# Performance work log

Hardware: AMD Instinct MI355X
Metric: run time of the kernel (lower is better)

The kernel has to match this reference:

```python
import jax, jax.numpy as jnp
import numpy as np

HIDDEN = 1024
ATT = 512

def _xavier(key, shape):
    fan_in, fan_out = shape[0], shape[1]
    bound = float(np.sqrt(6.0 / (fan_in + fan_out)))
    return jax.random.uniform(key, shape, jnp.float32, -bound, bound)

def setup_inputs() -> dict:
    key = jax.random.key(0)
    ks = jax.random.split(key, 7)
    B, P = 256, 196
    spatial_image = jax.random.normal(ks[0], (B, P, HIDDEN), jnp.float32)
    decoder_out = jax.random.normal(ks[1], (B, HIDDEN), jnp.float32)
    st = jax.random.normal(ks[2], (B, HIDDEN), jnp.float32)
    # weights stored as (in_dim, out_dim); math identical to torch Linear(x @ W.T)
    W_cnn = _xavier(ks[3], (HIDDEN, ATT))
    W_dec = _xavier(ks[4], (HIDDEN, ATT))
    W_sen = _xavier(ks[5], (HIDDEN, ATT))
    W_att = _xavier(ks[6], (ATT, 1))
    return {"spatial_image": spatial_image, "decoder_out": decoder_out, "st": st,
            "W_cnn": W_cnn, "W_dec": W_dec, "W_sen": W_sen, "W_att": W_att}

def reference(spatial_image, decoder_out, st, W_cnn, W_dec, W_sen, W_att):
    # dropout in eval mode (identity)
    cnn_out = jnp.einsum('bph,ha->bpa', spatial_image, W_cnn)   # (B,P,A)
    dec_out = decoder_out @ W_dec                                # (B,A)
    addition = jnp.tanh(cnn_out + dec_out[:, None, :])           # (B,P,A)
    zt = jnp.einsum('bpa,a->bp', addition, W_att[:, 0])          # (B,P)
    alpha_t = jax.nn.softmax(zt, axis=1)                         # (B,P)
    ct = jnp.einsum('bph,bp->bh', spatial_image, alpha_t)        # (B,H)
    sen = jnp.tanh(dec_out + st @ W_sen)                         # (B,A)
    out = sen @ W_att                                            # (B,1)
    concat = jnp.concatenate([zt, out], axis=1)                  # (B,P+1)
    alpha_hat = jax.nn.softmax(concat, axis=1)
    beta_t = alpha_hat[:, -1:]                                   # (B,1)
    c_hat = beta_t * st + (1.0 - beta_t) * ct                    # (B,H)
    return (alpha_t, beta_t, c_hat)
```

## Files before the change

### kernel.cpp

```cpp
#include <hip/hip_runtime.h>
#include <hip/hip_bf16.h>

#define BATCH   256
#define NP      196
#define HIDDEN  1024
#define ATT     512
#define M_TOTAL (BATCH * NP)

typedef __attribute__((ext_vector_type(8))) short bf16x8v;
typedef __attribute__((ext_vector_type(4))) float f32x4;

__device__ inline unsigned short f2bf(float x) {
    unsigned int u = __float_as_uint(x);
    u += 0x7fffu + ((u >> 16) & 1u);
    return (unsigned short)(u >> 16);
}

__device__ inline float fast_tanh(float x) {
    float e = __expf(2.0f * x);
    return 1.0f - 2.0f / (e + 1.0f);
}

__global__ void k0_arrange(const float* __restrict__ Wc, unsigned short* __restrict__ Wt) {
    int g = blockIdx.x * 256 + threadIdx.x;
    int kt    = g >> 11;
    int slot  = g & 2047;
    int chunk = slot >> 9;
    int n     = slot & 511;
    int kb = kt * 32 + chunk * 8;
    unsigned short v[8];
#pragma unroll
    for (int j = 0; j < 8; ++j) v[j] = f2bf(Wc[(kb + j) * ATT + n]);
    uint4 pk;
    pk.x = (unsigned int)v[0] | ((unsigned int)v[1] << 16);
    pk.y = (unsigned int)v[2] | ((unsigned int)v[3] << 16);
    pk.z = (unsigned int)v[4] | ((unsigned int)v[5] << 16);
    pk.w = (unsigned int)v[6] | ((unsigned int)v[7] << 16);
    *(uint4*)(Wt + (size_t)g * 8) = pk;
}

__global__ void k1_small(const float* __restrict__ dec_in, const float* __restrict__ st,
                         const float* __restrict__ Wdec,  const float* __restrict__ Wsen,
                         float* __restrict__ dec_out, float* __restrict__ stw) {
    const float* X = blockIdx.z ? st   : dec_in;
    const float* W = blockIdx.z ? Wsen : Wdec;
    float*       O = blockIdx.z ? stw  : dec_out;
    int ci = threadIdx.x & 31;
    int c0 = blockIdx.x * 128 + ci * 4;
    int b  = blockIdx.y * 8 + (threadIdx.x >> 5);
    const float* x = X + (size_t)b * HIDDEN;
    float4 acc = {0.f, 0.f, 0.f, 0.f};
    for (int k = 0; k < HIDDEN; k += 4) {
#pragma unroll
        for (int kk = 0; kk < 4; ++kk) {
            float4 w = *(const float4*)(W + (size_t)(k + kk) * ATT + c0);
            float a = x[k + kk];
            acc.x += a * w.x; acc.y += a * w.y; acc.z += a * w.z; acc.w += a * w.w;
        }
    }
    *(float4*)(O + (size_t)b * ATT + c0) = acc;
}

__global__ void __launch_bounds__(512)
k2_fused_gemm(const float* __restrict__ A, const unsigned short* __restrict__ Wt,
              const float* __restrict__ dec, const float* __restrict__ Watt,
              float* __restrict__ zt) {
    __shared__ __align__(16) unsigned short Abuf[4 * 64 * 8];
    __shared__ __align__(16) unsigned short Bbuf[4 * 512 * 8];
    __shared__ float zred[64 * 8];

    const int tid = threadIdx.x;
    const int w = tid >> 6;
    const int l = tid & 63;
    const int lg = l >> 4, ll = l & 15;
    const int r0 = blockIdx.x * 64;

    f32x4 acc[4][4];
#pragma unroll
    for (int m = 0; m < 4; ++m)
#pragma unroll
        for (int n = 0; n < 4; ++n) acc[m][n] = (f32x4){0.f, 0.f, 0.f, 0.f};

    const int arow = tid >> 3;
    const int akp  = tid & 7;
    const float* aptr = A + (size_t)(r0 + arow) * HIDDEN + akp * 4;
    const int aslot = (((akp >> 1) * 64 + arow) << 3) + (akp & 1) * 4;

    for (int kt = 0; kt < 32; ++kt) {
        float4 av = *(const float4*)(aptr + kt * 32);
        const uint4* bsrc = (const uint4*)(Wt + (size_t)kt * 16384);
        uint4 bv0 = bsrc[tid];
        uint4 bv1 = bsrc[512 + tid];
        uint4 bv2 = bsrc[1024 + tid];
        uint4 bv3 = bsrc[1536 + tid];

        __syncthreads();

        uint2 pk;
        pk.x = (unsigned int)f2bf(av.x) | ((unsigned int)f2bf(av.y) << 16);
        pk.y = (unsigned int)f2bf(av.z) | ((unsigned int)f2bf(av.w) << 16);
        *(uint2*)(Abuf + aslot) = pk;
        ((uint4*)Bbuf)[tid]        = bv0;
        ((uint4*)Bbuf)[512 + tid]  = bv1;
        ((uint4*)Bbuf)[1024 + tid] = bv2;
        ((uint4*)Bbuf)[1536 + tid] = bv3;

        __syncthreads();

        bf16x8v af[4], bfr[4];
#pragma unroll
        for (int m = 0; m < 4; ++m)
            af[m] = *(const bf16x8v*)(Abuf + ((lg * 64 + m * 16 + ll) << 3));
#pragma unroll
        for (int n = 0; n < 4; ++n)
            bfr[n] = *(const bf16x8v*)(Bbuf + ((lg * 512 + w * 64 + n * 16 + ll) << 3));
#pragma unroll
        for (int m = 0; m < 4; ++m)
#pragma unroll
            for (int n = 0; n < 4; ++n)
                acc[m][n] = __builtin_amdgcn_mfma_f32_16x16x32_bf16(af[m], bfr[n], acc[m][n], 0, 0, 0);
    }

    const int colb = w * 64 + ll;
    float watt[4];
#pragma unroll
    for (int n = 0; n < 4; ++n) watt[n] = Watt[colb + n * 16];

#pragma unroll
    for (int m = 0; m < 4; ++m) {
#pragma unroll
        for (int j = 0; j < 4; ++j) {
            int rl = m * 16 + lg * 4 + j;
            int rowg = r0 + rl;
            int b = rowg / NP;
            const float* db = dec + (size_t)b * ATT;
            float s = 0.f;
#pragma unroll
            for (int n = 0; n < 4; ++n)
                s += fast_tanh(acc[m][n][j] + db[colb + n * 16]) * watt[n];
            s += __shfl_xor(s, 1);
            s += __shfl_xor(s, 2);
            s += __shfl_xor(s, 4);
            s += __shfl_xor(s, 8);
            if (ll == 0) zred[rl * 8 + w] = s;
        }
    }
    __syncthreads();
    if (tid < 64) {
        float t = 0.f;
#pragma unroll
        for (int j = 0; j < 8; ++j) t += zred[tid * 8 + j];
        zt[r0 + tid] = t;
    }
}

__global__ void k3_softmax(const float* __restrict__ dec, const float* __restrict__ stw,
                           const float* __restrict__ Watt, const float* __restrict__ zt,
                           float* __restrict__ out, float* __restrict__ beta_ws) {
    int b = blockIdx.x;
    int t = threadIdx.x;
    __shared__ float red[256];

    float p = 0.f;
#pragma unroll
    for (int c = t; c < ATT; c += 256)
        p += fast_tanh(dec[(size_t)b * ATT + c] + stw[(size_t)b * ATT + c]) * Watt[c];
    red[t] = p;
    __syncthreads();
    for (int s = 128; s > 0; s >>= 1) { if (t < s) red[t] += red[t + s]; __syncthreads(); }
    float outv = red[0];
    __syncthreads();

    float z = (t < NP) ? zt[b * NP + t] : -1e30f;
    red[t] = z;
    __syncthreads();
    for (int s = 128; s > 0; s >>= 1) { if (t < s) red[t] = fmaxf(red[t], red[t + s]); __syncthreads(); }
    float m1 = red[0];
    __syncthreads();

    float e = (t < NP) ? __expf(z - m1) : 0.f;
    red[t] = e;
    __syncthreads();
    for (int s = 128; s > 0; s >>= 1) { if (t < s) red[t] += red[t + s]; __syncthreads(); }
    float s1 = red[0];

    if (t < NP) out[b * NP + t] = e / s1;

    if (t == 0) {
        float m2 = fmaxf(m1, outv);
        float s2 = s1 * __expf(m1 - m2) + __expf(outv - m2);
        float beta = __expf(outv - m2) / s2;
        out[M_TOTAL + b] = beta;
        beta_ws[b] = beta;
    }
}

__global__ void k4_ct(const float* __restrict__ spatial, const float* __restrict__ alpha,
                      float* __restrict__ ctp) {
    int q = blockIdx.x;
    int b = blockIdx.y;
    int t = threadIdx.x;
    __shared__ float al[49];
    if (t < 49) al[t] = alpha[b * NP + q * 49 + t];
    __syncthreads();
    const float* sp = spatial + (size_t)b * NP * HIDDEN + (size_t)q * 49 * HIDDEN + t * 4;
    float4 acc = {0.f, 0.f, 0.f, 0.f};
#pragma unroll 7
    for (int p = 0; p < 49; ++p) {
        float4 v = *(const float4*)(sp + (size_t)p * HIDDEN);
        float a = al[p];
        acc.x += a * v.x; acc.y += a * v.y; acc.z += a * v.z; acc.w += a * v.w;
    }
    *(float4*)(ctp + ((size_t)q * BATCH + b) * HIDDEN + t * 4) = acc;
}

__global__ void k5_chat(const float* __restrict__ st, const float* __restrict__ ctp,
                        const float* __restrict__ beta, float* __restrict__ chat) {
    int g = blockIdx.x * 256 + threadIdx.x;
    int b = g >> 8;
    int h0 = (g & 255) * 4;
    float be = beta[b];
    float4 s = *(const float4*)(st + (size_t)b * HIDDEN + h0);
    float4 c = {0.f, 0.f, 0.f, 0.f};
#pragma unroll
    for (int q = 0; q < 4; ++q) {
        float4 v = *(const float4*)(ctp + ((size_t)q * BATCH + b) * HIDDEN + h0);
        c.x += v.x; c.y += v.y; c.z += v.z; c.w += v.w;
    }
    float4 o;
    o.x = be * s.x + (1.f - be) * c.x;
    o.y = be * s.y + (1.f - be) * c.y;
    o.z = be * s.z + (1.f - be) * c.z;
    o.w = be * s.w + (1.f - be) * c.w;
    *(float4*)(chat + (size_t)b * HIDDEN + h0) = o;
}

extern "C" void kernel_launch(void* const* d_in, const int* in_sizes, int n_in,
                              void* d_out, int out_size, void* d_ws, size_t ws_size,
                              hipStream_t stream) {
    const float* spatial = (const float*)d_in[0];
    const float* decoder = (const float*)d_in[1];
    const float* st      = (const float*)d_in[2];
    const float* Wcnn    = (const float*)d_in[3];
    const float* Wdec    = (const float*)d_in[4];
    const float* Wsen    = (const float*)d_in[5];
    const float* Watt    = (const float*)d_in[6];
    float* out = (float*)d_out;

    char* ws = (char*)d_ws;
    unsigned short* Wt  = (unsigned short*)(ws + 0);
    float* zt   = (float*)(ws + 1048576);
    float* dec  = (float*)(ws + 1249280);
    float* stw  = (float*)(ws + 1773568);
    float* beta = (float*)(ws + 2297856);
    float* ctp  = (float*)(ws + 2298880);

    k0_arrange<<<256, 256, 0, stream>>>(Wcnn, Wt);
    k1_small<<<dim3(4, 32, 2), 256, 0, stream>>>(decoder, st, Wdec, Wsen, dec, stw);
    k2_fused_gemm<<<784, 512, 0, stream>>>(spatial, Wt, dec, Watt, zt);
    k3_softmax<<<256, 256, 0, stream>>>(dec, stw, Watt, zt, out, beta);
    k4_ct<<<dim3(4, 256), 256, 0, stream>>>(spatial, out, ctp);
    k5_chat<<<256, 256, 0, stream>>>(st, ctp, beta, out + M_TOTAL + BATCH);
}
```

Baseline: 192.5 us.

## Retile fused GEMM to 128x256 with direct-to-LDS B loads and split-N partial logits

The fused GEMM moves from 64-row tiles spanning all 512 attention columns to 128x256 tiles on a 2x4 wave grid. The weight is rearranged per column half, and partial logits for each half are written separately, then summed in the softmax kernel. B tiles go straight from global memory to LDS via global_load_lds. A loads are prefetched one k-step ahead and converted with a packed bf16 instruction. A block-index swizzle groups tiles for L2 locality. The intent is less LDS staging traffic, more A reuse per weight load, and latency hiding, at the cost of an extra partial-logit buffer and tighter occupancy bounds.

```diff
diff --git a/kernel.cpp b/kernel.cpp
--- a/kernel.cpp
+++ b/kernel.cpp
@@ -6,6 +6,11 @@
 #define HIDDEN  1024
 #define ATT     512
 #define M_TOTAL (BATCH * NP)
+#define BM 128
+#define BN 256
+#define BK 32
+#define MT_TILES (M_TOTAL / BM)
+#define NB_TILES (ATT / BN)
 
 typedef __attribute__((ext_vector_type(8))) short bf16x8v;
 typedef __attribute__((ext_vector_type(4))) float f32x4;
@@ -16,21 +21,36 @@
     return (unsigned short)(u >> 16);
 }
 
+__device__ __forceinline__ unsigned int pk2bf(float lo, float hi) {
+    unsigned int r;
+    asm("v_cvt_pk_bf16_f32 %0, %1, %2" : "=v"(r) : "v"(lo), "v"(hi));
+    return r;
+}
+
 __device__ inline float fast_tanh(float x) {
     float e = __expf(2.0f * x);
     return 1.0f - 2.0f / (e + 1.0f);
 }
 
+__device__ __forceinline__ void glds16(const void* gsrc, void* ldst) {
+    __builtin_amdgcn_global_load_lds(
+        (const __attribute__((address_space(1))) unsigned int*)gsrc,
+        (__attribute__((address_space(3))) unsigned int*)ldst,
+        16, 0, 0);
+}
+
 __global__ void k0_arrange(const float* __restrict__ Wc, unsigned short* __restrict__ Wt) {
     int g = blockIdx.x * 256 + threadIdx.x;
-    int kt    = g >> 11;
-    int slot  = g & 2047;
-    int chunk = slot >> 9;
-    int n     = slot & 511;
-    int kb = kt * 32 + chunk * 8;
+    int nb    = g >> 15;
+    int rem   = g & 32767;
+    int kt    = rem >> 10;
+    int chunk = (rem >> 8) & 3;
+    int n     = rem & 255;
+    int col   = nb * 256 + n;
+    int kb    = kt * 32 + chunk * 8;
     unsigned short v[8];
 #pragma unroll
-    for (int j = 0; j < 8; ++j) v[j] = f2bf(Wc[(kb + j) * ATT + n]);
+    for (int j = 0; j < 8; ++j) v[j] = f2bf(Wc[(size_t)(kb + j) * ATT + col]);
     uint4 pk;
     pk.x = (unsigned int)v[0] | ((unsigned int)v[1] << 16);
     pk.y = (unsigned int)v[2] | ((unsigned int)v[3] << 16);
@@ -61,19 +81,25 @@
     *(float4*)(O + (size_t)b * ATT + c0) = acc;
 }
 
-__global__ void __launch_bounds__(512)
+__global__ void __launch_bounds__(512, 4)
 k2_fused_gemm(const float* __restrict__ A, const unsigned short* __restrict__ Wt,
               const float* __restrict__ dec, const float* __restrict__ Watt,
-              float* __restrict__ zt) {
-    __shared__ __align__(16) unsigned short Abuf[4 * 64 * 8];
-    __shared__ __align__(16) unsigned short Bbuf[4 * 512 * 8];
-    __shared__ float zred[64 * 8];
+              float* __restrict__ ztp) {
+    __shared__ __align__(16) unsigned short Abuf[4 * 128 * 8];
+    __shared__ __align__(16) unsigned short Bbuf[4 * 256 * 8];
+    __shared__ float zred[128 * 4];
 
     const int tid = threadIdx.x;
-    const int w = tid >> 6;
-    const int l = tid & 63;
+    const int w  = tid >> 6;
+    const int l  = tid & 63;
     const int lg = l >> 4, ll = l & 15;
-    const int r0 = blockIdx.x * 64;
+    const int wr = w >> 2, wc = w & 3;
+
+    const int bid = (int)blockIdx.x;
+    const int swz = (bid & 7) * 98 + (bid >> 3);
+    const int mt = swz >> 1, nb = swz & 1;
+    const int r0 = mt * BM;
+    const int c0 = nb * BN;
 
     f32x4 acc[4][4];
 #pragma unroll
@@ -81,39 +107,47 @@
 #pragma unroll
         for (int n = 0; n < 4; ++n) acc[m][n] = (f32x4){0.f, 0.f, 0.f, 0.f};
 
-    const int arow = tid >> 3;
-    const int akp  = tid & 7;
-    const float* aptr = A + (size_t)(r0 + arow) * HIDDEN + akp * 4;
-    const int aslot = (((akp >> 1) * 64 + arow) << 3) + (akp & 1) * 4;
+    const int arow = tid >> 2;
+    const int ach  = tid & 3;
+    const float* aptr = A + (size_t)(r0 + arow) * HIDDEN + ach * 8;
+    unsigned short* aslot = Abuf + (ach * 128 + arow) * 8;
+
+    const size_t wt_base = (size_t)nb * 32 * 8192;
+    const char* bsrc0 = (const char*)(Wt + wt_base) + (w * 2 + 0) * 1024 + l * 16;
+    const char* bsrc1 = (const char*)(Wt + wt_base) + (w * 2 + 1) * 1024 + l * 16;
+    char* bdst0 = (char*)Bbuf + (w * 2 + 0) * 1024 + l * 16;
+    char* bdst1 = (char*)Bbuf + (w * 2 + 1) * 1024 + l * 16;
+
+    float4 a0 = *(const float4*)(aptr);
+    float4 a1 = *(const float4*)(aptr + 4);
 
     for (int kt = 0; kt < 32; ++kt) {
-        float4 av = *(const float4*)(aptr + kt * 32);
-        const uint4* bsrc = (const uint4*)(Wt + (size_t)kt * 16384);
-        uint4 bv0 = bsrc[tid];
-        uint4 bv1 = bsrc[512 + tid];
-        uint4 bv2 = bsrc[1024 + tid];
-        uint4 bv3 = bsrc[1536 + tid];
-
         __syncthreads();
 
-        uint2 pk;
-        pk.x = (unsigned int)f2bf(av.x) | ((unsigned int)f2bf(av.y) << 16);
-        pk.y = (unsigned int)f2bf(av.z) | ((unsigned int)f2bf(av.w) << 16);
-        *(uint2*)(Abuf + aslot) = pk;
-        ((uint4*)Bbuf)[tid]        = bv0;
-        ((uint4*)Bbuf)[512 + tid]  = bv1;
-        ((uint4*)Bbuf)[1024 + tid] = bv2;
-        ((uint4*)Bbuf)[1536 + tid] = bv3;
+        glds16(bsrc0 + kt * 16384, bdst0);
+        glds16(bsrc1 + kt * 16384, bdst1);
+
+        uint4 ap;
+        ap.x = pk2bf(a0.x, a0.y);
+        ap.y = pk2bf(a0.z, a0.w);
+        ap.z = pk2bf(a1.x, a1.y);
+        ap.w = pk2bf(a1.z, a1.w);
+        *(uint4*)aslot = ap;
 
         __syncthreads();
 
+        if (kt < 31) {
+            a0 = *(const float4*)(aptr + (kt + 1) * 32);
+            a1 = *(const float4*)(aptr + (kt + 1) * 32 + 4);
+        }
+
         bf16x8v af[4], bfr[4];
 #pragma unroll
         for (int m = 0; m < 4; ++m)
-            af[m] = *(const bf16x8v*)(Abuf + ((lg * 64 + m * 16 + ll) << 3));
+            af[m] = *(const bf16x8v*)(Abuf + ((lg * 128 + wr * 64 + m * 16 + ll) << 3));
 #pragma unroll
         for (int n = 0; n < 4; ++n)
-            bfr[n] = *(const bf16x8v*)(Bbuf + ((lg * 512 + w * 64 + n * 16 + ll) << 3));
+            bfr[n] = *(const bf16x8v*)(Bbuf + ((lg * 256 + wc * 64 + n * 16 + ll) << 3));
 #pragma unroll
         for (int m = 0; m < 4; ++m)
 #pragma unroll
@@ -121,41 +155,39 @@
                 acc[m][n] = __builtin_amdgcn_mfma_f32_16x16x32_bf16(af[m], bfr[n], acc[m][n], 0, 0, 0);
     }
 
-    const int colb = w * 64 + ll;
+    const int clocal = wc * 64 + ll;
     float watt[4];
 #pragma unroll
-    for (int n = 0; n < 4; ++n) watt[n] = Watt[colb + n * 16];
+    for (int n = 0; n < 4; ++n) watt[n] = Watt[c0 + clocal + n * 16];
 
 #pragma unroll
     for (int m = 0; m < 4; ++m) {
 #pragma unroll
         for (int j = 0; j < 4; ++j) {
-            int rl = m * 16 + lg * 4 + j;
+            int rl = wr * 64 + m * 16 + lg * 4 + j;
             int rowg = r0 + rl;
             int b = rowg / NP;
-            const float* db = dec + (size_t)b * ATT;
+            const float* db = dec + (size_t)b * ATT + c0;
             float s = 0.f;
 #pragma unroll
             for (int n = 0; n < 4; ++n)
-                s += fast_tanh(acc[m][n][j] + db[colb + n * 16]) * watt[n];
+                s += fast_tanh(acc[m][n][j] + db[clocal + n * 16]) * watt[n];
             s += __shfl_xor(s, 1);
             s += __shfl_xor(s, 2);
             s += __shfl_xor(s, 4);
             s += __shfl_xor(s, 8);
-            if (ll == 0) zred[rl * 8 + w] = s;
+            if (ll == 0) zred[rl * 4 + wc] = s;
         }
     }
     __syncthreads();
-    if (tid < 64) {
-        float t = 0.f;
-#pragma unroll
-        for (int j = 0; j < 8; ++j) t += zred[tid * 8 + j];
-        zt[r0 + tid] = t;
+    if (tid < 128) {
+        float t = zred[tid * 4] + zred[tid * 4 + 1] + zred[tid * 4 + 2] + zred[tid * 4 + 3];
+        ztp[(size_t)nb * M_TOTAL + r0 + tid] = t;
     }
 }
 
 __global__ void k3_softmax(const float* __restrict__ dec, const float* __restrict__ stw,
-                           const float* __restrict__ Watt, const float* __restrict__ zt,
+                           const float* __restrict__ Watt, const float* __restrict__ ztp,
                            float* __restrict__ out, float* __restrict__ beta_ws) {
     int b = blockIdx.x;
     int t = threadIdx.x;
@@ -171,7 +203,8 @@
     float outv = red[0];
     __syncthreads();
 
-    float z = (t < NP) ? zt[b * NP + t] : -1e30f;
+    float z = -1e30f;
+    if (t < NP) z = ztp[b * NP + t] + ztp[M_TOTAL + b * NP + t];
     red[t] = z;
     __syncthreads();
     for (int s = 128; s > 0; s >>= 1) { if (t < s) red[t] = fmaxf(red[t], red[t + s]); __syncthreads(); }
@@ -248,17 +281,17 @@
     float* out = (float*)d_out;
 
     char* ws = (char*)d_ws;
-    unsigned short* Wt  = (unsigned short*)(ws + 0);
-    float* zt   = (float*)(ws + 1048576);
-    float* dec  = (float*)(ws + 1249280);
-    float* stw  = (float*)(ws + 1773568);
-    float* beta = (float*)(ws + 2297856);
-    float* ctp  = (float*)(ws + 2298880);
+    unsigned short* Wt = (unsigned short*)(ws + 0);
+    float* ztp  = (float*)(ws + 1048576);
+    float* dec  = (float*)(ws + 1449984);
+    float* stw  = (float*)(ws + 1974272);
+    float* beta = (float*)(ws + 2498560);
+    float* ctp  = (float*)(ws + 2499584);
 
     k0_arrange<<<256, 256, 0, stream>>>(Wcnn, Wt);
     k1_small<<<dim3(4, 32, 2), 256, 0, stream>>>(decoder, st, Wdec, Wsen, dec, stw);
-    k2_fused_gemm<<<784, 512, 0, stream>>>(spatial, Wt, dec, Watt, zt);
-    k3_softmax<<<256, 256, 0, stream>>>(dec, stw, Watt, zt, out, beta);
+    k2_fused_gemm<<<MT_TILES * NB_TILES, 512, 0, stream>>>(spatial, Wt, dec, Watt, ztp);
+    k3_softmax<<<256, 256, 0, stream>>>(dec, stw, Watt, ztp, out, beta);
     k4_ct<<<dim3(4, 256), 256, 0, stream>>>(spatial, out, ctp);
     k5_chat<<<256, 256, 0, stream>>>(st, ctp, beta, out + M_TOTAL + BATCH);
 }
```

Result: faster. 186.2 us (-3.3%).

## Restructure fused GEMM: resident A tile in LDS, double-buffered async B loads

Applied to the files above, without the earlier changes.

The main GEMM kernel now loads the full 64x1024 A row tile once, converts it to bf16 with packed conversions, and keeps it resident in a swizzled 128KB LDS region. The N dimension is split into two 256-column halves processed sequentially by 4 waves, and B tiles are streamed with global_load_lds into double buffers so loads overlap MFMA work. It also adds a block-index remap, XOR swizzles to avoid bank conflicts, and s_setprio around MFMAs. The aim is to remove per-iteration A reloads and register-staged B copies, at the cost of one block per CU due to the large LDS footprint.

```diff
diff --git a/kernel.cpp b/kernel.cpp
--- a/kernel.cpp
+++ b/kernel.cpp
@@ -6,6 +6,8 @@
 #define HIDDEN  1024
 #define ATT     512
 #define M_TOTAL (BATCH * NP)
+#define BM 64
+#define MT_TILES (M_TOTAL / BM)
 
 typedef __attribute__((ext_vector_type(8))) short bf16x8v;
 typedef __attribute__((ext_vector_type(4))) float f32x4;
@@ -16,21 +18,36 @@
     return (unsigned short)(u >> 16);
 }
 
+__device__ __forceinline__ unsigned int pk2bf(float lo, float hi) {
+    unsigned int r;
+    asm("v_cvt_pk_bf16_f32 %0, %1, %2" : "=v"(r) : "v"(lo), "v"(hi));
+    return r;
+}
+
 __device__ inline float fast_tanh(float x) {
     float e = __expf(2.0f * x);
     return 1.0f - 2.0f / (e + 1.0f);
 }
 
+__device__ __forceinline__ void glds16(const void* gsrc, void* ldst) {
+    __builtin_amdgcn_global_load_lds(
+        (const __attribute__((address_space(1))) unsigned int*)gsrc,
+        (__attribute__((address_space(3))) unsigned int*)ldst,
+        16, 0, 0);
+}
+
 __global__ void k0_arrange(const float* __restrict__ Wc, unsigned short* __restrict__ Wt) {
     int g = blockIdx.x * 256 + threadIdx.x;
-    int kt    = g >> 11;
-    int slot  = g & 2047;
-    int chunk = slot >> 9;
-    int n     = slot & 511;
-    int kb = kt * 32 + chunk * 8;
+    int h    = g >> 15;
+    int kt   = (g >> 10) & 31;
+    int col  = (g >> 2) & 255;
+    int slot = g & 3;
+    int c    = slot ^ ((col >> 1) & 3);
+    int kb   = kt * 32 + c * 8;
+    int colg = h * 256 + col;
     unsigned short v[8];
 #pragma unroll
-    for (int j = 0; j < 8; ++j) v[j] = f2bf(Wc[(kb + j) * ATT + n]);
+    for (int j = 0; j < 8; ++j) v[j] = f2bf(Wc[(size_t)(kb + j) * ATT + colg]);
     uint4 pk;
     pk.x = (unsigned int)v[0] | ((unsigned int)v[1] << 16);
     pk.y = (unsigned int)v[2] | ((unsigned int)v[3] << 16);
@@ -61,96 +78,152 @@
     *(float4*)(O + (size_t)b * ATT + c0) = acc;
 }
 
-__global__ void __launch_bounds__(512)
-k2_fused_gemm(const float* __restrict__ A, const unsigned short* __restrict__ Wt,
-              const float* __restrict__ dec, const float* __restrict__ Watt,
-              float* __restrict__ zt) {
-    __shared__ __align__(16) unsigned short Abuf[4 * 64 * 8];
-    __shared__ __align__(16) unsigned short Bbuf[4 * 512 * 8];
-    __shared__ float zred[64 * 8];
+__global__ void __launch_bounds__(256, 1)
+k2_fused(const float* __restrict__ A, const unsigned short* __restrict__ Wt,
+         const float* __restrict__ dec, const float* __restrict__ Watt,
+         float* __restrict__ zt) {
+    __shared__ __align__(16) char lds[163840];
+    char* B0 = lds + 131072;
+    char* B1 = lds + 147456;
+    float* zred = (float*)(lds + 131072);
 
     const int tid = threadIdx.x;
-    const int w = tid >> 6;
-    const int l = tid & 63;
+    const int wv = tid >> 6;
+    const int l  = tid & 63;
     const int lg = l >> 4, ll = l & 15;
-    const int r0 = blockIdx.x * 64;
+
+    const int bid = (int)blockIdx.x;
+    const int mt = (bid & 7) * 98 + (bid >> 3);
+    const int r0 = mt * BM;
 
     f32x4 acc[4][4];
 #pragma unroll
     for (int m = 0; m < 4; ++m)
 #pragma unroll
         for (int n = 0; n < 4; ++n) acc[m][n] = (f32x4){0.f, 0.f, 0.f, 0.f};
-
-    const int arow = tid >> 3;
-    const int akp  = tid & 7;
-    const float* aptr = A + (size_t)(r0 + arow) * HIDDEN + akp * 4;
-    const int aslot = (((akp >> 1) * 64 + arow) << 3) + (akp & 1) * 4;
-
-    for (int kt = 0; kt < 32; ++kt) {
-        float4 av = *(const float4*)(aptr + kt * 32);
-        const uint4* bsrc = (const uint4*)(Wt + (size_t)kt * 16384);
-        uint4 bv0 = bsrc[tid];
-        uint4 bv1 = bsrc[512 + tid];
-        uint4 bv2 = bsrc[1024 + tid];
-        uint4 bv3 = bsrc[1536 + tid];
-
-        __syncthreads();
-
-        uint2 pk;
-        pk.x = (unsigned int)f2bf(av.x) | ((unsigned int)f2bf(av.y) << 16);
-        pk.y = (unsigned int)f2bf(av.z) | ((unsigned int)f2bf(av.w) << 16);
-        *(uint2*)(Abuf + aslot) = pk;
-        ((uint4*)Bbuf)[tid]        = bv0;
-        ((uint4*)Bbuf)[512 + tid]  = bv1;
-        ((uint4*)Bbuf)[1024 + tid] = bv2;
-        ((uint4*)Bbuf)[1536 + tid] = bv3;
-
-        __syncthreads();
-
-        bf16x8v af[4], bfr[4];
+    float srow[4][4];
+#pragma unroll
+    for (int m = 0; m < 4; ++m)
+#pragma unroll
+        for (int j = 0; j < 4; ++j) srow[m][j] = 0.f;
+
+    const float* Asrc = A + (size_t)r0 * HIDDEN;
+
+#define BSTAGE(h, kt, Bb) do {                                                 \
+    const char* _s = (const char*)Wt + (size_t)(h) * 524288 +                  \
+                     (size_t)(kt) * 16384 + tid * 16;                          \
+    glds16(_s,          (Bb) + tid * 16);                                      \
+    glds16(_s + 4096,   (Bb) + 4096  + tid * 16);                              \
+    glds16(_s + 8192,   (Bb) + 8192  + tid * 16);                              \
+    glds16(_s + 12288,  (Bb) + 12288 + tid * 16);                              \
+} while (0)
+
+#define COMPUTE(t, Bb) do {                                                    \
+    bf16x8v af[4], bfr[4];                                                     \
+    _Pragma("unroll")                                                          \
+    for (int m = 0; m < 4; ++m) {                                              \
+        int row = m * 16 + ll;                                                 \
+        af[m] = *(const bf16x8v*)(lds + row * 2048 +                           \
+                 (((t) * 64 + (lg << 4)) ^ ((row & 7) << 4)));                 \
+    }                                                                          \
+    _Pragma("unroll")                                                          \
+    for (int n = 0; n < 4; ++n) {                                              \
+        int col = wv * 64 + n * 16 + ll;                                       \
+        bfr[n] = *(const bf16x8v*)((Bb) + col * 64 +                           \
+                 (((lg << 4)) ^ (((col >> 1) & 3) << 4)));                     \
+    }                                                                          \
+    __builtin_amdgcn_s_setprio(1);                                             \
+    _Pragma("unroll")                                                          \
+    for (int m = 0; m < 4; ++m)                                                \
+        _Pragma("unroll")                                                      \
+        for (int n = 0; n < 4; ++n)                                            \
+            acc[m][n] = __builtin_amdgcn_mfma_f32_16x16x32_bf16(               \
+                af[m], bfr[n], acc[m][n], 0, 0, 0);                            \
+    __builtin_amdgcn_s_setprio(0);                                             \
+} while (0)
+
+#define SYNCV do {                                                             \
+    asm volatile("s_waitcnt vmcnt(0)" ::: "memory");                           \
+    __builtin_amdgcn_s_barrier();                                              \
+} while (0)
+
+    BSTAGE(0, 0, B0);
+#pragma unroll
+    for (int bb = 0; bb < 4; ++bb) {
+        float4 tt[16];
+#pragma unroll
+        for (int i2 = 0; i2 < 16; ++i2)
+            tt[i2] = *(const float4*)(Asrc + ((size_t)(bb * 16 + i2) * 256 + tid) * 4);
+#pragma unroll
+        for (int i2 = 0; i2 < 16; ++i2) {
+            int i = bb * 16 + i2;
+            uint2 u;
+            u.x = pk2bf(tt[i2].x, tt[i2].y);
+            u.y = pk2bf(tt[i2].z, tt[i2].w);
+            *(uint2*)(lds + i * 2048 + ((tid * 8) ^ ((i & 7) << 4))) = u;
+        }
+    }
+    asm volatile("s_waitcnt vmcnt(0) lgkmcnt(0)" ::: "memory");
+    __builtin_amdgcn_s_barrier();
+
+#pragma unroll 1
+    for (int h = 0; h < 2; ++h) {
+        for (int tp = 0; tp < 15; ++tp) {
+            const int t = tp * 2;
+            BSTAGE(h, t + 1, B1); COMPUTE(t, B0); SYNCV;
+            BSTAGE(h, t + 2, B0); COMPUTE(t + 1, B1); SYNCV;
+        }
+        BSTAGE(h, 31, B1); COMPUTE(30, B0); SYNCV;
+        if (h == 0) { BSTAGE(1, 0, B0); COMPUTE(31, B1); SYNCV; }
+        else        { COMPUTE(31, B1); }
+
+        const int clocal = wv * 64 + ll;
+        const int cg = h * 256 + clocal;
+        float watt[4];
+#pragma unroll
+        for (int n = 0; n < 4; ++n) watt[n] = Watt[cg + n * 16];
+#pragma unroll
+        for (int m = 0; m < 4; ++m) {
+#pragma unroll
+            for (int j = 0; j < 4; ++j) {
+                int rowg = r0 + m * 16 + lg * 4 + j;
+                int b = rowg / NP;
+                const float* db = dec + (size_t)b * ATT + cg;
+                float s = 0.f;
+#pragma unroll
+                for (int n = 0; n < 4; ++n)
+                    s += fast_tanh(acc[m][n][j] + db[n * 16]) * watt[n];
+                s += __shfl_xor(s, 1);
+                s += __shfl_xor(s, 2);
+                s += __shfl_xor(s, 4);
+                s += __shfl_xor(s, 8);
+                srow[m][j] += s;
+            }
+        }
+        if (h == 0) {
+#pragma unroll
+            for (int m = 0; m < 4; ++m)
+#pragma unroll
+                for (int n = 0; n < 4; ++n) acc[m][n] = (f32x4){0.f, 0.f, 0.f, 0.f};
+        }
+    }
+
+#undef BSTAGE
+#undef COMPUTE
+#undef SYNCV
+
+    __builtin_amdgcn_s_barrier();
+    if (ll == 0) {
 #pragma unroll
         for (int m = 0; m < 4; ++m)
-            af[m] = *(const bf16x8v*)(Abuf + ((lg * 64 + m * 16 + ll) << 3));
-#pragma unroll
-        for (int n = 0; n < 4; ++n)
-            bfr[n] = *(const bf16x8v*)(Bbuf + ((lg * 512 + w * 64 + n * 16 + ll) << 3));
-#pragma unroll
-        for (int m = 0; m < 4; ++m)
-#pragma unroll
-            for (int n = 0; n < 4; ++n)
-                acc[m][n] = __builtin_amdgcn_mfma_f32_16x16x32_bf16(af[m], bfr[n], acc[m][n], 0, 0, 0);
-    }
-
-    const int colb = w * 64 + ll;
-    float watt[4];
-#pragma unroll
-    for (int n = 0; n < 4; ++n) watt[n] = Watt[colb + n * 16];
-
-#pragma unroll
-    for (int m = 0; m < 4; ++m) {
-#pragma unroll
-        for (int j = 0; j < 4; ++j) {
-            int rl = m * 16 + lg * 4 + j;
-            int rowg = r0 + rl;
-            int b = rowg / NP;
-            const float* db = dec + (size_t)b * ATT;
-            float s = 0.f;
-#pragma unroll
-            for (int n = 0; n < 4; ++n)
-                s += fast_tanh(acc[m][n][j] + db[colb + n * 16]) * watt[n];
-            s += __shfl_xor(s, 1);
-            s += __shfl_xor(s, 2);
-            s += __shfl_xor(s, 4);
-            s += __shfl_xor(s, 8);
-            if (ll == 0) zred[rl * 8 + w] = s;
-        }
+#pragma unroll
+            for (int j = 0; j < 4; ++j)
+                zred[(m * 16 + lg * 4 + j) * 4 + wv] = srow[m][j];
     }
     __syncthreads();
     if (tid < 64) {
-        float t = 0.f;
-#pragma unroll
-        for (int j = 0; j < 8; ++j) t += zred[tid * 8 + j];
-        zt[r0 + tid] = t;
+        zt[r0 + tid] = zred[tid * 4] + zred[tid * 4 + 1]
+                     + zred[tid * 4 + 2] + zred[tid * 4 + 3];
     }
 }
 
@@ -248,7 +321,7 @@
     float* out = (float*)d_out;
 
     char* ws = (char*)d_ws;
-    unsigned short* Wt  = (unsigned short*)(ws + 0);
+    unsigned short* Wt = (unsigned short*)(ws + 0);
     float* zt   = (float*)(ws + 1048576);
     float* dec  = (float*)(ws + 1249280);
     float* stw  = (float*)(ws + 1773568);
@@ -257,7 +330,7 @@
 
     k0_arrange<<<256, 256, 0, stream>>>(Wcnn, Wt);
     k1_small<<<dim3(4, 32, 2), 256, 0, stream>>>(decoder, st, Wdec, Wsen, dec, stw);
-    k2_fused_gemm<<<784, 512, 0, stream>>>(spatial, Wt, dec, Watt, zt);
+    k2_fused<<<MT_TILES, 256, 0, stream>>>(spatial, Wt, dec, Watt, zt);
     k3_softmax<<<256, 256, 0, stream>>>(dec, stw, Watt, zt, out, beta);
     k4_ct<<<dim3(4, 256), 256, 0, stream>>>(spatial, out, ctp);
     k5_chat<<<256, 256, 0, stream>>>(st, ctp, beta, out + M_TOTAL + BATCH);
```

Measured after the change: 279.2 us. +45.1%, slower.
